# Kernel optimization log

Hardware: AMD Instinct MI355X
Metric: run time of the kernel (lower is better)

Reference implementation:

```python
import jax, jax.numpy as jnp
import numpy as np

WH, WW = 16, 16          # window size
NUM_HEADS = 6
DIM = 192
N = WH * WW              # tokens per window

def _rel_coords_table():
    # (2*WH-1, 2*WW-1, 2), normalized and scaled by 8 (Swin-V2 style)
    rch = np.arange(-(WH - 1), WH, dtype=np.float32)
    rcw = np.arange(-(WW - 1), WW, dtype=np.float32)
    tab = np.stack(np.meshgrid(rch, rcw, indexing='ij'), axis=-1)
    tab[..., 0] /= (WH - 1)
    tab[..., 1] /= (WW - 1)
    tab *= 8.0
    return tab

def _rel_pos_index():
    # (N, N) int indices into the flattened bias table
    coords = np.stack(np.meshgrid(np.arange(WH), np.arange(WW), indexing='ij'))  # (2,WH,WW)
    cf = coords.reshape(2, -1)                                                   # (2,N)
    rel = cf[:, :, None] - cf[:, None, :]                                        # (2,N,N)
    rel = rel.transpose(1, 2, 0).astype(np.int64)                                # (N,N,2)
    rel[..., 0] += WH - 1
    rel[..., 1] += WW - 1
    rel[..., 0] *= 2 * WW - 1
    return rel.sum(-1)                                                           # (N,N)

_TABLE = jnp.asarray(_rel_coords_table())          # (2WH-1, 2WW-1, 2)
_INDEX = jnp.asarray(_rel_pos_index().reshape(-1)) # (N*N,)

def setup_inputs() -> dict:
    key = jax.random.key(0)
    ks = jax.random.split(key, 8)
    B_ = 256  # num_windows(64) * batch(4)
    return {
        'x': jax.random.normal(ks[0], (B_, N, DIM), dtype=jnp.float32),
        'scale': jax.random.uniform(ks[1], (1, 2), dtype=jnp.float32),
        'mask': jnp.zeros((64, N, N), dtype=jnp.float32),
        'qkv_w': jax.random.normal(ks[2], (3 * DIM, DIM), dtype=jnp.float32) * 0.02,
        'qkv_b': jnp.zeros((3 * DIM,), dtype=jnp.float32),
        'cpb_w1': jax.random.normal(ks[3], (512, 4), dtype=jnp.float32) * 0.02,
        'cpb_b1': jnp.zeros((512,), dtype=jnp.float32),
        'cpb_w2': jax.random.normal(ks[4], (NUM_HEADS, 512), dtype=jnp.float32) * 0.02,
        'cpb_b2': jnp.zeros((NUM_HEADS,), dtype=jnp.float32),
        'proj_w': jax.random.normal(ks[5], (DIM, DIM), dtype=jnp.float32) * 0.02,
        'proj_b': jnp.zeros((DIM,), dtype=jnp.float32),
    }

def reference(x, scale, mask, qkv_w, qkv_b, cpb_w1, cpb_b1, cpb_w2, cpb_b2, proj_w, proj_b):
    B_, n, C = x.shape
    H = NUM_HEADS
    hd = C // H
    qk_scale = hd ** -0.5

    qkv = x @ qkv_w.T + qkv_b                       # (B_, N, 3C)
    qkv = qkv.reshape(B_, n, 3, H, hd).transpose(2, 0, 3, 1, 4)
    q, k, v = qkv[0], qkv[1], qkv[2]                # each (B_, H, N, hd)

    attn = jnp.einsum('bhnd,bhmd->bhnm', q * qk_scale, k)  # (B_, H, N, N)

    # continuous relative position bias: concat table with broadcast scale -> MLP
    rel_cell = jnp.broadcast_to(scale[0], _TABLE.shape[:2] + (2,))    # (2WH-1,2WW-1,2)
    coords4 = jnp.concatenate([_TABLE, rel_cell], axis=-1)            # (...,4)
    hmid = jax.nn.relu(coords4 @ cpb_w1.T + cpb_b1)                   # (...,512)
    table = (hmid @ cpb_w2.T + cpb_b2).reshape(-1, H)                 # (M, H)
    bias = table[_INDEX].reshape(n, n, H).transpose(2, 0, 1)          # (H, N, N)

    attn = attn + bias[None]
    nW = mask.shape[0]
    attn = attn.reshape(B_ // nW, nW, H, n, n) + mask[None, :, None]
    attn = attn.reshape(B_, H, n, n)
    attn = jax.nn.softmax(attn, axis=-1)

    out = jnp.einsum('bhnm,bhmd->bhnd', attn, v)    # (B_, H, N, hd)
    out = out.transpose(0, 2, 1, 3).reshape(B_, n, C)
    return out @ proj_w.T + proj_b
```

## Files before the change

kernel.cpp:

```cpp
#include <hip/hip_runtime.h>
#include <math.h>

#define N_TOK 256
#define NHEADS 6
#define DIM_C 192
#define HD 32
#define B_WIN 256

typedef short bf16x8 __attribute__((ext_vector_type(8)));
typedef float f32x4 __attribute__((ext_vector_type(4)));

__device__ inline short f2bf(float f) {
    unsigned u = __float_as_uint(f);
    u = (u + 0x7fffu + ((u >> 16) & 1u)) >> 16;
    return (short)u;
}
__device__ inline short f2bf_fast(float f) {
    return (short)((__float_as_uint(f) + 0x8000u) >> 16);
}
__device__ inline float bf2f(short s) {
    return __uint_as_float(((unsigned)(unsigned short)s) << 16);
}

__global__ __launch_bounds__(512) void cpb_table_kernel(
    const float* __restrict__ scale, const float* __restrict__ w1,
    const float* __restrict__ b1, const float* __restrict__ w2,
    const float* __restrict__ b2, float* __restrict__ table)
{
    __shared__ float red[512];
    const int e = blockIdx.x;
    const int i = e / 31, j = e % 31;
    const float t0 = ((float)(i - 15)) * (8.0f / 15.0f);
    const float t1 = ((float)(j - 15)) * (8.0f / 15.0f);
    const float s0 = scale[0], s1 = scale[1];
    const int t = threadIdx.x;
    const float* w = w1 + t * 4;
    float h = w[0] * t0 + w[1] * t1 + w[2] * s0 + w[3] * s1 + b1[t];
    h = fmaxf(h, 0.0f);
    for (int head = 0; head < NHEADS; ++head) {
        red[t] = h * w2[head * 512 + t];
        __syncthreads();
        for (int s = 256; s > 0; s >>= 1) {
            if (t < s) red[t] += red[t + s];
            __syncthreads();
        }
        if (t == 0) table[e * NHEADS + head] = red[0] + b2[head];
        __syncthreads();
    }
}


__global__ __launch_bounds__(256) void bias_perm_kernel(
    const float* __restrict__ table, short* __restrict__ bias_p)
{
    const int idx8 = blockIdx.x * 256 + threadIdx.x;
    const int h = idx8 >> 13;
    const int rem = idx8 & 8191;
    const int rb = rem >> 9;
    const int g = (rem >> 6) & 7;
    const int lane = rem & 63;
    const int quad = lane >> 4, l15 = lane & 15;
    bf16x8 o;
#pragma unroll
    for (int j = 0; j < 8; ++j) {
        const int nt = g * 2 + (j >> 2), r = j & 3;
        const int row = rb * 16 + quad * 4 + r;
        const int col = nt * 16 + l15;
        const int rel0 = (row >> 4) - (col >> 4) + 15;
        const int rel1 = (row & 15) - (col & 15) + 15;
        o[j] = f2bf(table[(rel0 * 31 + rel1) * NHEADS + h]);
    }
    ((bf16x8*)bias_p)[idx8] = o;
}

__global__ __launch_bounds__(256) void mask_perm_kernel(
    const float* __restrict__ mask, short* __restrict__ mask_p)
{
    const int idx8 = blockIdx.x * 256 + threadIdx.x;
    const int bw = idx8 >> 13;
    const int rem = idx8 & 8191;
    const int rb = rem >> 9;
    const int g = (rem >> 6) & 7;
    const int lane = rem & 63;
    const int quad = lane >> 4, l15 = lane & 15;
    const float* ms = mask + ((size_t)bw << 16);
    bf16x8 o;
#pragma unroll
    for (int j = 0; j < 8; ++j) {
        const int nt = g * 2 + (j >> 2), r = j & 3;
        const int row = rb * 16 + quad * 4 + r;
        const int col = nt * 16 + l15;
        o[j] = f2bf(ms[row * 256 + col]);
    }
    ((bf16x8*)mask_p)[idx8] = o;
}

__global__ __launch_bounds__(256) void f32_to_bf16_kernel(
    const float* __restrict__ in, short* __restrict__ out, int n4)
{
    const int i = blockIdx.x * 256 + threadIdx.x;
    if (i < n4) {
        float4 v = ((const float4*)in)[i];
        short4 s;
        s.x = f2bf(v.x); s.y = f2bf(v.y); s.z = f2bf(v.z); s.w = f2bf(v.w);
        ((short4*)out)[i] = s;
    }
}

__global__ __launch_bounds__(256) void qkv_gemm_kernel(
    const short* __restrict__ x16, const short* __restrict__ w16,
    const float* __restrict__ qkv_b,
    short* __restrict__ qb, short* __restrict__ kb, short* __restrict__ vb)
{
    const int t = threadIdx.x;
    const int lane = t & 63;
    const int w = t >> 6;
    const int l15 = lane & 15, quad = lane >> 4;
    const int n0 = blockIdx.x * 64;
    const int m0 = blockIdx.y * 128 + w * 32;

    f32x4 acc[2][4] = {};
#pragma unroll
    for (int ks = 0; ks < 6; ++ks) {
        bf16x8 af[2];
#pragma unroll
        for (int mt = 0; mt < 2; ++mt)
            af[mt] = *(const bf16x8*)(x16 + (size_t)(m0 + mt * 16 + l15) * DIM_C + ks * 32 + quad * 8);
        bf16x8 bfr[4];
#pragma unroll
        for (int nt = 0; nt < 4; ++nt)
            bfr[nt] = *(const bf16x8*)(w16 + (size_t)(n0 + nt * 16 + l15) * DIM_C + ks * 32 + quad * 8);
#pragma unroll
        for (int mt = 0; mt < 2; ++mt)
#pragma unroll
            for (int nt = 0; nt < 4; ++nt)
                acc[mt][nt] = __builtin_amdgcn_mfma_f32_16x16x32_bf16(af[mt], bfr[nt], acc[mt][nt], 0, 0, 0);
    }

    const int which = n0 / DIM_C;
    short* outp = (which == 0) ? qb : (which == 1) ? kb : vb;
    const float qscale = (which == 0) ? 0.17677669529663689f : 1.0f;
#pragma unroll
    for (int mt = 0; mt < 2; ++mt) {
#pragma unroll
        for (int r = 0; r < 4; ++r) {
            const int m = m0 + mt * 16 + quad * 4 + r;
            const int b = m >> 8, tok = m & 255;
#pragma unroll
            for (int nt = 0; nt < 4; ++nt) {
                const int c = n0 + nt * 16 + l15;
                const int rem = c - which * DIM_C;
                const int h = rem >> 5, d = rem & 31;
                const float val = (acc[mt][nt][r] + qkv_b[c]) * qscale;
                outp[((size_t)((b * NHEADS + h) * N_TOK + tok)) * HD + d] = f2bf(val);
            }
        }
    }
}

__global__ __launch_bounds__(256) void proj_gemm_kernel(
    const short* __restrict__ A16, const short* __restrict__ w16,
    const float* __restrict__ proj_b, float* __restrict__ out)
{
    const int t = threadIdx.x;
    const int lane = t & 63;
    const int w = t >> 6;
    const int l15 = lane & 15, quad = lane >> 4;
    const int n0 = blockIdx.x * 64;
    const int m0 = blockIdx.y * 128 + w * 32;

    f32x4 acc[2][4] = {};
#pragma unroll
    for (int ks = 0; ks < 6; ++ks) {
        bf16x8 af[2];
#pragma unroll
        for (int mt = 0; mt < 2; ++mt)
            af[mt] = *(const bf16x8*)(A16 + (size_t)(m0 + mt * 16 + l15) * DIM_C + ks * 32 + quad * 8);
        bf16x8 bfr[4];
#pragma unroll
        for (int nt = 0; nt < 4; ++nt)
            bfr[nt] = *(const bf16x8*)(w16 + (size_t)(n0 + nt * 16 + l15) * DIM_C + ks * 32 + quad * 8);
#pragma unroll
        for (int mt = 0; mt < 2; ++mt)
#pragma unroll
            for (int nt = 0; nt < 4; ++nt)
                acc[mt][nt] = __builtin_amdgcn_mfma_f32_16x16x32_bf16(af[mt], bfr[nt], acc[mt][nt], 0, 0, 0);
    }

#pragma unroll
    for (int mt = 0; mt < 2; ++mt) {
#pragma unroll
        for (int r = 0; r < 4; ++r) {
            const int m = m0 + mt * 16 + quad * 4 + r;
#pragma unroll
            for (int nt = 0; nt < 4; ++nt) {
                const int c = n0 + nt * 16 + l15;
                out[(size_t)m * DIM_C + c] = acc[mt][nt][r] + proj_b[c];
            }
        }
    }
}

#define PS_LD 264

__global__ __launch_bounds__(256, 3) void attn_mfma_kernel(
    const short* __restrict__ q, const short* __restrict__ k,
    const short* __restrict__ v, const short* __restrict__ bias_p,
    const short* __restrict__ mask_p, short* __restrict__ out16)
{
    __shared__ __align__(16) short Vt[32][PS_LD];
    __shared__ __align__(16) short Pw[4][16][PS_LD];

    const int l = blockIdx.x;
    const int s = l >> 3;
    const int bw = (l & 7) + 8 * (s / 24);
    const int j = s % 24;
    const int h = j % 6;
    const int b = (j / 6) * 64 + bw;

    const int t = threadIdx.x;
    const int lane = t & 63;
    const int w = t >> 6;
    const int l15 = lane & 15;
    const int quad = lane >> 4;
    const size_t slab = ((size_t)(b * NHEADS + h)) * (N_TOK * HD);

    {
        const bf16x8* vrow = (const bf16x8*)(v + slab + (size_t)t * HD);
#pragma unroll
        for (int u = 0; u < 4; ++u) {
            bf16x8 vv = vrow[u];
#pragma unroll
            for (int jj = 0; jj < 8; ++jj) {
                const int d = u * 8 + jj;
                Vt[d][t ^ (((d >> 3) & 1) * 16)] = vv[jj];
            }
        }
    }

    bf16x8 kfr[16];
#pragma unroll
    for (int nt = 0; nt < 16; ++nt)
        kfr[nt] = *(const bf16x8*)(k + slab + (size_t)(nt * 16 + l15) * HD + quad * 8);

    __syncthreads();

    const short* bslab = bias_p + h * 65536;
    const short* mslab = mask_p + bw * 65536;

    for (int chunk = 0; chunk < 4; ++chunk) {
        const int rb = chunk * 4 + w;

        const bf16x8 qf = *(const bf16x8*)(q + slab + (size_t)(rb * 16 + l15) * HD + quad * 8);

        f32x4 S[16];
#pragma unroll
        for (int half = 0; half < 2; ++half) {
            bf16x8 bb[4], mm[4];
#pragma unroll
            for (int gg = 0; gg < 4; ++gg) {
                const int g = half * 4 + gg;
                const int off = ((rb * 8 + g) * 64 + lane) * 8;
                bb[gg] = *(const bf16x8*)(bslab + off);
                mm[gg] = *(const bf16x8*)(mslab + off);
            }
#pragma unroll
            for (int gg = 0; gg < 4; ++gg) {
                const int g = half * 4 + gg;
                f32x4 c0, c1;
#pragma unroll
                for (int r = 0; r < 4; ++r) {
                    c0[r] = bf2f(bb[gg][r])     + bf2f(mm[gg][r]);
                    c1[r] = bf2f(bb[gg][4 + r]) + bf2f(mm[gg][4 + r]);
                }
                S[g * 2]     = __builtin_amdgcn_mfma_f32_16x16x32_bf16(qf, kfr[g * 2],     c0, 0, 0, 0);
                S[g * 2 + 1] = __builtin_amdgcn_mfma_f32_16x16x32_bf16(qf, kfr[g * 2 + 1], c1, 0, 0, 0);
            }
        }

        float mx[4] = {-1e30f, -1e30f, -1e30f, -1e30f};
#pragma unroll
        for (int nt = 0; nt < 16; ++nt)
#pragma unroll
            for (int r = 0; r < 4; ++r)
                mx[r] = fmaxf(mx[r], S[nt][r]);
#pragma unroll
        for (int r = 0; r < 4; ++r) {
            mx[r] = fmaxf(mx[r], __shfl_xor(mx[r], 1));
            mx[r] = fmaxf(mx[r], __shfl_xor(mx[r], 2));
            mx[r] = fmaxf(mx[r], __shfl_xor(mx[r], 4));
            mx[r] = fmaxf(mx[r], __shfl_xor(mx[r], 8));
        }

        float sm[4] = {0.f, 0.f, 0.f, 0.f};
#pragma unroll
        for (int nt = 0; nt < 16; ++nt) {
#pragma unroll
            for (int r = 0; r < 4; ++r) {
                const float p = __expf(S[nt][r] - mx[r]);
                sm[r] += p;
                const int lr = quad * 4 + r;
                Pw[w][lr][(nt * 16 + l15) ^ (((lr >> 3) & 1) * 16)] = f2bf_fast(p);
            }
        }
        float inv[4];
#pragma unroll
        for (int r = 0; r < 4; ++r) {
            sm[r] += __shfl_xor(sm[r], 1);
            sm[r] += __shfl_xor(sm[r], 2);
            sm[r] += __shfl_xor(sm[r], 4);
            sm[r] += __shfl_xor(sm[r], 8);
            inv[r] = __builtin_amdgcn_rcpf(sm[r]);
        }

        __asm__ volatile("s_waitcnt lgkmcnt(0)" ::: "memory");

        f32x4 O0 = {0.f, 0.f, 0.f, 0.f};
        f32x4 O1 = {0.f, 0.f, 0.f, 0.f};
        const int sw = ((l15 >> 3) & 1) * 16;
#pragma unroll
        for (int ks = 0; ks < 8; ++ks) {
            const int cb = ks * 32 + quad * 8;
            bf16x8 af  = *(const bf16x8*)&Pw[w][l15][cb ^ sw];
            bf16x8 bf0 = *(const bf16x8*)&Vt[l15][cb ^ sw];
            bf16x8 bf1 = *(const bf16x8*)&Vt[16 + l15][cb ^ sw];
            O0 = __builtin_amdgcn_mfma_f32_16x16x32_bf16(af, bf0, O0, 0, 0, 0);
            O1 = __builtin_amdgcn_mfma_f32_16x16x32_bf16(af, bf1, O1, 0, 0, 0);
        }

#pragma unroll
        for (int r = 0; r < 4; ++r) {
            const int token = rb * 16 + quad * 4 + r;
            short* dst = out16 + ((size_t)(b * N_TOK + token)) * DIM_C + h * HD;
            dst[l15]      = f2bf_fast(O0[r] * inv[r]);
            dst[16 + l15] = f2bf_fast(O1[r] * inv[r]);
        }
    }
}

extern "C" void kernel_launch(void* const* d_in, const int* in_sizes, int n_in,
                              void* d_out, int out_size, void* d_ws, size_t ws_size,
                              hipStream_t stream)
{
    const float* x      = (const float*)d_in[0];
    const float* scale  = (const float*)d_in[1];
    const float* mask   = (const float*)d_in[2];
    const float* qkv_w  = (const float*)d_in[3];
    const float* qkv_b  = (const float*)d_in[4];
    const float* cpb_w1 = (const float*)d_in[5];
    const float* cpb_b1 = (const float*)d_in[6];
    const float* cpb_w2 = (const float*)d_in[7];
    const float* cpb_b2 = (const float*)d_in[8];
    const float* proj_w = (const float*)d_in[9];
    const float* proj_b = (const float*)d_in[10];
    float* out = (float*)d_out;

    const size_t per = (size_t)B_WIN * NHEADS * N_TOK * HD;
    short* wss     = (short*)d_ws;
    short* qb      = wss;
    short* kb      = qb + per;
    short* vb      = kb + per;
    short* ao      = vb + per;
    short* x16     = ao + per;
    short* bias_p  = x16 + per;
    short* mask_p  = bias_p + 393216;
    short* qkvw16  = mask_p + 4194304;
    short* projw16 = qkvw16 + 110592;
    float* table   = (float*)(projw16 + 36864);

    cpb_table_kernel<<<961, 512, 0, stream>>>(scale, cpb_w1, cpb_b1, cpb_w2, cpb_b2, table);

    bias_perm_kernel<<<(NHEADS * 8192) / 256, 256, 0, stream>>>(table, bias_p);
    mask_perm_kernel<<<(64 * 8192) / 256, 256, 0, stream>>>(mask, mask_p);

    f32_to_bf16_kernel<<<(int)((per / 4 + 255) / 256), 256, 0, stream>>>(x, x16, (int)(per / 4));
    f32_to_bf16_kernel<<<(110592 / 4 + 255) / 256, 256, 0, stream>>>(qkv_w, qkvw16, 110592 / 4);
    f32_to_bf16_kernel<<<(36864 / 4 + 255) / 256, 256, 0, stream>>>(proj_w, projw16, 36864 / 4);

    qkv_gemm_kernel<<<dim3(9, 512), 256, 0, stream>>>(x16, qkvw16, qkv_b, qb, kb, vb);

    attn_mfma_kernel<<<NHEADS * B_WIN, 256, 0, stream>>>(qb, kb, vb, bias_p, mask_p, ao);

    proj_gemm_kernel<<<dim3(3, 512), 256, 0, stream>>>(ao, projw16, proj_b, out);
}
```

Measured before the change: 330.7 us.

## Fuse x bf16 conversion into QKV GEMM and stage row tiles in LDS

The QKV GEMM now reads fp32 x directly, converts a 64-row tile to bf16 in shared memory and loops over all output column tiles, so the separate x conversion kernel is dropped. The projection GEMM is restructured the same way, staging its A rows in LDS and reusing them across all column tiles. This removes a full round trip of x through global memory and repeated A reads across column blocks. In exchange there are fewer, longer blocks (1024) with serialized column loops, less parallelism per block, and an added LDS barrier.

```diff
diff --git a/kernel.cpp b/kernel.cpp
--- a/kernel.cpp
+++ b/kernel.cpp
@@ -108,50 +108,60 @@
 }
 
 __global__ __launch_bounds__(256) void qkv_gemm_kernel(
-    const short* __restrict__ x16, const short* __restrict__ w16,
+    const float* __restrict__ x, const short* __restrict__ w16,
     const float* __restrict__ qkv_b,
     short* __restrict__ qb, short* __restrict__ kb, short* __restrict__ vb)
 {
+    __shared__ __align__(16) short A[64][200];
     const int t = threadIdx.x;
     const int lane = t & 63;
     const int w = t >> 6;
     const int l15 = lane & 15, quad = lane >> 4;
-    const int n0 = blockIdx.x * 64;
-    const int m0 = blockIdx.y * 128 + w * 32;
-
-    f32x4 acc[2][4] = {};
-#pragma unroll
-    for (int ks = 0; ks < 6; ++ks) {
-        bf16x8 af[2];
-#pragma unroll
-        for (int mt = 0; mt < 2; ++mt)
-            af[mt] = *(const bf16x8*)(x16 + (size_t)(m0 + mt * 16 + l15) * DIM_C + ks * 32 + quad * 8);
-        bf16x8 bfr[4];
-#pragma unroll
-        for (int nt = 0; nt < 4; ++nt)
-            bfr[nt] = *(const bf16x8*)(w16 + (size_t)(n0 + nt * 16 + l15) * DIM_C + ks * 32 + quad * 8);
-#pragma unroll
-        for (int mt = 0; mt < 2; ++mt)
-#pragma unroll
-            for (int nt = 0; nt < 4; ++nt)
-                acc[mt][nt] = __builtin_amdgcn_mfma_f32_16x16x32_bf16(af[mt], bfr[nt], acc[mt][nt], 0, 0, 0);
-    }
-
-    const int which = n0 / DIM_C;
-    short* outp = (which == 0) ? qb : (which == 1) ? kb : vb;
-    const float qscale = (which == 0) ? 0.17677669529663689f : 1.0f;
-#pragma unroll
-    for (int mt = 0; mt < 2; ++mt) {
-#pragma unroll
-        for (int r = 0; r < 4; ++r) {
-            const int m = m0 + mt * 16 + quad * 4 + r;
+    const int m0 = blockIdx.x * 64;
+
+    {
+        const int row = t >> 2, p = t & 3;
+        const float4* src = (const float4*)(x + (size_t)(m0 + row) * DIM_C + p * 48);
+#pragma unroll
+        for (int j = 0; j < 6; ++j) {
+            float4 v0 = src[j * 2];
+            float4 v1 = src[j * 2 + 1];
+            bf16x8 o;
+            o[0] = f2bf(v0.x); o[1] = f2bf(v0.y); o[2] = f2bf(v0.z); o[3] = f2bf(v0.w);
+            o[4] = f2bf(v1.x); o[5] = f2bf(v1.y); o[6] = f2bf(v1.z); o[7] = f2bf(v1.w);
+            *(bf16x8*)&A[row][p * 48 + j * 8] = o;
+        }
+    }
+    __syncthreads();
+
+    const int rowA = w * 16 + l15;
+
+    for (int nt = 0; nt < 9; ++nt) {
+        const int n0 = nt * 64;
+        f32x4 acc[4] = {};
+#pragma unroll
+        for (int ks = 0; ks < 6; ++ks) {
+            const bf16x8 af = *(const bf16x8*)&A[rowA][ks * 32 + quad * 8];
+#pragma unroll
+            for (int c4 = 0; c4 < 4; ++c4) {
+                const bf16x8 bfr = *(const bf16x8*)(w16 + (size_t)(n0 + c4 * 16 + l15) * DIM_C + ks * 32 + quad * 8);
+                acc[c4] = __builtin_amdgcn_mfma_f32_16x16x32_bf16(af, bfr, acc[c4], 0, 0, 0);
+            }
+        }
+
+        const int which = nt / 3;
+        short* outp = (which == 0) ? qb : (which == 1) ? kb : vb;
+        const float qscale = (which == 0) ? 0.17677669529663689f : 1.0f;
+#pragma unroll
+        for (int r = 0; r < 4; ++r) {
+            const int m = m0 + w * 16 + quad * 4 + r;
             const int b = m >> 8, tok = m & 255;
 #pragma unroll
-            for (int nt = 0; nt < 4; ++nt) {
-                const int c = n0 + nt * 16 + l15;
+            for (int c4 = 0; c4 < 4; ++c4) {
+                const int c = n0 + c4 * 16 + l15;
                 const int rem = c - which * DIM_C;
                 const int h = rem >> 5, d = rem & 31;
-                const float val = (acc[mt][nt][r] + qkv_b[c]) * qscale;
+                const float val = (acc[c4][r] + qkv_b[c]) * qscale;
                 outp[((size_t)((b * NHEADS + h) * N_TOK + tok)) * HD + d] = f2bf(val);
             }
         }
@@ -162,40 +172,44 @@
     const short* __restrict__ A16, const short* __restrict__ w16,
     const float* __restrict__ proj_b, float* __restrict__ out)
 {
+    __shared__ __align__(16) short A[64][200];
     const int t = threadIdx.x;
     const int lane = t & 63;
     const int w = t >> 6;
     const int l15 = lane & 15, quad = lane >> 4;
-    const int n0 = blockIdx.x * 64;
-    const int m0 = blockIdx.y * 128 + w * 32;
-
-    f32x4 acc[2][4] = {};
-#pragma unroll
-    for (int ks = 0; ks < 6; ++ks) {
-        bf16x8 af[2];
-#pragma unroll
-        for (int mt = 0; mt < 2; ++mt)
-            af[mt] = *(const bf16x8*)(A16 + (size_t)(m0 + mt * 16 + l15) * DIM_C + ks * 32 + quad * 8);
-        bf16x8 bfr[4];
-#pragma unroll
-        for (int nt = 0; nt < 4; ++nt)
-            bfr[nt] = *(const bf16x8*)(w16 + (size_t)(n0 + nt * 16 + l15) * DIM_C + ks * 32 + quad * 8);
-#pragma unroll
-        for (int mt = 0; mt < 2; ++mt)
-#pragma unroll
-            for (int nt = 0; nt < 4; ++nt)
-                acc[mt][nt] = __builtin_amdgcn_mfma_f32_16x16x32_bf16(af[mt], bfr[nt], acc[mt][nt], 0, 0, 0);
-    }
-
-#pragma unroll
-    for (int mt = 0; mt < 2; ++mt) {
-#pragma unroll
-        for (int r = 0; r < 4; ++r) {
-            const int m = m0 + mt * 16 + quad * 4 + r;
-#pragma unroll
-            for (int nt = 0; nt < 4; ++nt) {
-                const int c = n0 + nt * 16 + l15;
-                out[(size_t)m * DIM_C + c] = acc[mt][nt][r] + proj_b[c];
+    const int m0 = blockIdx.x * 64;
+
+    {
+        const int row = t >> 2, p = t & 3;
+        const bf16x8* src = (const bf16x8*)(A16 + (size_t)(m0 + row) * DIM_C + p * 48);
+#pragma unroll
+        for (int j = 0; j < 6; ++j)
+            *(bf16x8*)&A[row][p * 48 + j * 8] = src[j];
+    }
+    __syncthreads();
+
+    const int rowA = w * 16 + l15;
+
+#pragma unroll
+    for (int nt = 0; nt < 3; ++nt) {
+        const int n0 = nt * 64;
+        f32x4 acc[4] = {};
+#pragma unroll
+        for (int ks = 0; ks < 6; ++ks) {
+            const bf16x8 af = *(const bf16x8*)&A[rowA][ks * 32 + quad * 8];
+#pragma unroll
+            for (int c4 = 0; c4 < 4; ++c4) {
+                const bf16x8 bfr = *(const bf16x8*)(w16 + (size_t)(n0 + c4 * 16 + l15) * DIM_C + ks * 32 + quad * 8);
+                acc[c4] = __builtin_amdgcn_mfma_f32_16x16x32_bf16(af, bfr, acc[c4], 0, 0, 0);
+            }
+        }
+#pragma unroll
+        for (int r = 0; r < 4; ++r) {
+            const int m = m0 + w * 16 + quad * 4 + r;
+#pragma unroll
+            for (int c4 = 0; c4 < 4; ++c4) {
+                const int c = n0 + c4 * 16 + l15;
+                out[(size_t)m * DIM_C + c] = acc[c4][r] + proj_b[c];
             }
         }
     }
@@ -373,13 +387,12 @@
     bias_perm_kernel<<<(NHEADS * 8192) / 256, 256, 0, stream>>>(table, bias_p);
     mask_perm_kernel<<<(64 * 8192) / 256, 256, 0, stream>>>(mask, mask_p);
 
-    f32_to_bf16_kernel<<<(int)((per / 4 + 255) / 256), 256, 0, stream>>>(x, x16, (int)(per / 4));
     f32_to_bf16_kernel<<<(110592 / 4 + 255) / 256, 256, 0, stream>>>(qkv_w, qkvw16, 110592 / 4);
     f32_to_bf16_kernel<<<(36864 / 4 + 255) / 256, 256, 0, stream>>>(proj_w, projw16, 36864 / 4);
 
-    qkv_gemm_kernel<<<dim3(9, 512), 256, 0, stream>>>(x16, qkvw16, qkv_b, qb, kb, vb);
+    qkv_gemm_kernel<<<1024, 256, 0, stream>>>(x, qkvw16, qkv_b, qb, kb, vb);
 
     attn_mfma_kernel<<<NHEADS * B_WIN, 256, 0, stream>>>(qb, kb, vb, bias_p, mask_p, ao);
 
-    proj_gemm_kernel<<<dim3(3, 512), 256, 0, stream>>>(ao, projw16, proj_b, out);
-}
+    proj_gemm_kernel<<<1024, 256, 0, stream>>>(ao, projw16, proj_b, out);
+}
```

Result: slower. 362.2 us (+9.5%).

## Fuse x fp32-to-bf16 conversion into QKV GEMM and remap blocks per XCD

Applied to the files above, without the earlier changes.

Removes the separate kernel that converted x to bf16. The QKV GEMM now loads fp32 x directly and packs it to bf16 with v_cvt_pk_bf16_f32, which saves a full write and re-read of the bf16 copy of x. Both GEMMs switch to a 1D grid that is remapped so that all column tiles of an M panel land on the same XCD, improving L2 reuse of the A rows. The cost is that each x element is now read as fp32 and converted 9 times (once per column tile), which doubles A-load bytes inside the GEMM.

```diff
diff --git a/kernel.cpp b/kernel.cpp
--- a/kernel.cpp
+++ b/kernel.cpp
@@ -20,6 +20,11 @@
 }
 __device__ inline float bf2f(short s) {
     return __uint_as_float(((unsigned)(unsigned short)s) << 16);
+}
+__device__ inline unsigned cvt_pk_bf16(float lo, float hi) {
+    unsigned r;
+    asm("v_cvt_pk_bf16_f32 %0, %1, %2" : "=v"(r) : "v"(lo), "v"(hi));
+    return r;
 }
 
 __global__ __launch_bounds__(512) void cpb_table_kernel(
@@ -108,7 +113,7 @@
 }
 
 __global__ __launch_bounds__(256) void qkv_gemm_kernel(
-    const short* __restrict__ x16, const short* __restrict__ w16,
+    const float* __restrict__ x, const short* __restrict__ w16,
     const float* __restrict__ qkv_b,
     short* __restrict__ qb, short* __restrict__ kb, short* __restrict__ vb)
 {
@@ -116,28 +121,43 @@
     const int lane = t & 63;
     const int w = t >> 6;
     const int l15 = lane & 15, quad = lane >> 4;
-    const int n0 = blockIdx.x * 64;
-    const int m0 = blockIdx.y * 128 + w * 32;
+
+    const int l = blockIdx.x;
+    const int xcd = l & 7;
+    const int s = l >> 3;
+    const int nt = s % 9;
+    const int panel = xcd + 8 * (s / 9);
+    const int m0 = panel * 128 + w * 32;
+    const int n0 = nt * 64;
 
     f32x4 acc[2][4] = {};
 #pragma unroll
     for (int ks = 0; ks < 6; ++ks) {
         bf16x8 af[2];
 #pragma unroll
+        for (int mt = 0; mt < 2; ++mt) {
+            const float* ap = x + (size_t)(m0 + mt * 16 + l15) * DIM_C + ks * 32 + quad * 8;
+            const float4 v0 = *(const float4*)ap;
+            const float4 v1 = *(const float4*)(ap + 4);
+            union { bf16x8 v; unsigned u[4]; } cv;
+            cv.u[0] = cvt_pk_bf16(v0.x, v0.y);
+            cv.u[1] = cvt_pk_bf16(v0.z, v0.w);
+            cv.u[2] = cvt_pk_bf16(v1.x, v1.y);
+            cv.u[3] = cvt_pk_bf16(v1.z, v1.w);
+            af[mt] = cv.v;
+        }
+        bf16x8 bfr[4];
+#pragma unroll
+        for (int c4 = 0; c4 < 4; ++c4)
+            bfr[c4] = *(const bf16x8*)(w16 + (size_t)(n0 + c4 * 16 + l15) * DIM_C + ks * 32 + quad * 8);
+#pragma unroll
         for (int mt = 0; mt < 2; ++mt)
-            af[mt] = *(const bf16x8*)(x16 + (size_t)(m0 + mt * 16 + l15) * DIM_C + ks * 32 + quad * 8);
-        bf16x8 bfr[4];
-#pragma unroll
-        for (int nt = 0; nt < 4; ++nt)
-            bfr[nt] = *(const bf16x8*)(w16 + (size_t)(n0 + nt * 16 + l15) * DIM_C + ks * 32 + quad * 8);
-#pragma unroll
-        for (int mt = 0; mt < 2; ++mt)
-#pragma unroll
-            for (int nt = 0; nt < 4; ++nt)
-                acc[mt][nt] = __builtin_amdgcn_mfma_f32_16x16x32_bf16(af[mt], bfr[nt], acc[mt][nt], 0, 0, 0);
-    }
-
-    const int which = n0 / DIM_C;
+#pragma unroll
+            for (int c4 = 0; c4 < 4; ++c4)
+                acc[mt][c4] = __builtin_amdgcn_mfma_f32_16x16x32_bf16(af[mt], bfr[c4], acc[mt][c4], 0, 0, 0);
+    }
+
+    const int which = nt / 3;
     short* outp = (which == 0) ? qb : (which == 1) ? kb : vb;
     const float qscale = (which == 0) ? 0.17677669529663689f : 1.0f;
 #pragma unroll
@@ -147,11 +167,11 @@
             const int m = m0 + mt * 16 + quad * 4 + r;
             const int b = m >> 8, tok = m & 255;
 #pragma unroll
-            for (int nt = 0; nt < 4; ++nt) {
-                const int c = n0 + nt * 16 + l15;
+            for (int c4 = 0; c4 < 4; ++c4) {
+                const int c = n0 + c4 * 16 + l15;
                 const int rem = c - which * DIM_C;
                 const int h = rem >> 5, d = rem & 31;
-                const float val = (acc[mt][nt][r] + qkv_b[c]) * qscale;
+                const float val = (acc[mt][c4][r] + qkv_b[c]) * qscale;
                 outp[((size_t)((b * NHEADS + h) * N_TOK + tok)) * HD + d] = f2bf(val);
             }
         }
@@ -166,8 +186,14 @@
     const int lane = t & 63;
     const int w = t >> 6;
     const int l15 = lane & 15, quad = lane >> 4;
-    const int n0 = blockIdx.x * 64;
-    const int m0 = blockIdx.y * 128 + w * 32;
+
+    const int l = blockIdx.x;
+    const int xcd = l & 7;
+    const int s = l >> 3;
+    const int nt = s % 3;
+    const int panel = xcd + 8 * (s / 3);
+    const int m0 = panel * 128 + w * 32;
+    const int n0 = nt * 64;
 
     f32x4 acc[2][4] = {};
 #pragma unroll
@@ -178,13 +204,13 @@
             af[mt] = *(const bf16x8*)(A16 + (size_t)(m0 + mt * 16 + l15) * DIM_C + ks * 32 + quad * 8);
         bf16x8 bfr[4];
 #pragma unroll
-        for (int nt = 0; nt < 4; ++nt)
-            bfr[nt] = *(const bf16x8*)(w16 + (size_t)(n0 + nt * 16 + l15) * DIM_C + ks * 32 + quad * 8);
+        for (int c4 = 0; c4 < 4; ++c4)
+            bfr[c4] = *(const bf16x8*)(w16 + (size_t)(n0 + c4 * 16 + l15) * DIM_C + ks * 32 + quad * 8);
 #pragma unroll
         for (int mt = 0; mt < 2; ++mt)
 #pragma unroll
-            for (int nt = 0; nt < 4; ++nt)
-                acc[mt][nt] = __builtin_amdgcn_mfma_f32_16x16x32_bf16(af[mt], bfr[nt], acc[mt][nt], 0, 0, 0);
+            for (int c4 = 0; c4 < 4; ++c4)
+                acc[mt][c4] = __builtin_amdgcn_mfma_f32_16x16x32_bf16(af[mt], bfr[c4], acc[mt][c4], 0, 0, 0);
     }
 
 #pragma unroll
@@ -193,9 +219,9 @@
         for (int r = 0; r < 4; ++r) {
             const int m = m0 + mt * 16 + quad * 4 + r;
 #pragma unroll
-            for (int nt = 0; nt < 4; ++nt) {
-                const int c = n0 + nt * 16 + l15;
-                out[(size_t)m * DIM_C + c] = acc[mt][nt][r] + proj_b[c];
+            for (int c4 = 0; c4 < 4; ++c4) {
+                const int c = n0 + c4 * 16 + l15;
+                out[(size_t)m * DIM_C + c] = acc[mt][c4][r] + proj_b[c];
             }
         }
     }
@@ -373,13 +399,12 @@
     bias_perm_kernel<<<(NHEADS * 8192) / 256, 256, 0, stream>>>(table, bias_p);
     mask_perm_kernel<<<(64 * 8192) / 256, 256, 0, stream>>>(mask, mask_p);
 
-    f32_to_bf16_kernel<<<(int)((per / 4 + 255) / 256), 256, 0, stream>>>(x, x16, (int)(per / 4));
     f32_to_bf16_kernel<<<(110592 / 4 + 255) / 256, 256, 0, stream>>>(qkv_w, qkvw16, 110592 / 4);
     f32_to_bf16_kernel<<<(36864 / 4 + 255) / 256, 256, 0, stream>>>(proj_w, projw16, 36864 / 4);
 
-    qkv_gemm_kernel<<<dim3(9, 512), 256, 0, stream>>>(x16, qkvw16, qkv_b, qb, kb, vb);
+    qkv_gemm_kernel<<<4608, 256, 0, stream>>>(x, qkvw16, qkv_b, qb, kb, vb);
 
     attn_mfma_kernel<<<NHEADS * B_WIN, 256, 0, stream>>>(qb, kb, vb, bias_p, mask_p, ao);
 
-    proj_gemm_kernel<<<dim3(3, 512), 256, 0, stream>>>(ao, projw16, proj_b, out);
-}
+    proj_gemm_kernel<<<1536, 256, 0, stream>>>(ao, projw16, proj_b, out);
+}
```

New measurement: 347.8 us. +5.2%, slower.
